# Kernel tuning notes

Hardware: AMD Instinct MI355X
Metric: run time of the kernel (lower is better)

## Reference

```python
import jax, jax.numpy as jnp
import numpy as np
from jax import lax

DIM = 192
HEADS = 6

def conv1x1(x, w, b):
    # x: [B,C,H,W], w: [O,C], b: [O]
    return jnp.einsum('oc,bchw->bohw', w, x) + b[None, :, None, None]

def dwconv3x3(x, w, b):
    # x: [B,C,H,W], w: [C,1,3,3] depthwise
    y = lax.conv_general_dilated(x, w, window_strides=(1, 1), padding='SAME',
                                 feature_group_count=x.shape[1],
                                 dimension_numbers=('NCHW', 'OIHW', 'NCHW'))
    return y + b[None, :, None, None]

def l2norm(x, eps=1e-12):
    # normalize along last axis (matches torch F.normalize)
    n = jnp.sqrt(jnp.sum(x * x, axis=-1, keepdims=True))
    return x / jnp.maximum(n, eps)

def setup_inputs() -> dict:
    key = jax.random.key(0)
    ks = jax.random.split(key, 12)
    b, c, h, w = 8, DIM, 128, 128
    s = 0.02
    return {
        'hsi': jax.random.normal(ks[0], (b, c, h, w), jnp.float32),
        'lidar': jax.random.normal(ks[1], (b, c, h, w), jnp.float32),
        'hsi_qv_w': jax.random.normal(ks[2], (2 * c, c), jnp.float32) * s,
        'hsi_qv_b': jnp.zeros((2 * c,), jnp.float32),
        'lidar_kv_w': jax.random.normal(ks[3], (2 * c, c), jnp.float32) * s,
        'lidar_kv_b': jnp.zeros((2 * c,), jnp.float32),
        'hsi_dw_w': jax.random.normal(ks[4], (2 * c, 1, 3, 3), jnp.float32) * s,
        'hsi_dw_b': jnp.zeros((2 * c,), jnp.float32),
        'lidar_dw_w': jax.random.normal(ks[5], (2 * c, 1, 3, 3), jnp.float32) * s,
        'lidar_dw_b': jnp.zeros((2 * c,), jnp.float32),
        'temperature': jnp.ones((HEADS, 1, 1), jnp.float32),
    }

def reference(hsi, lidar, hsi_qv_w, hsi_qv_b, lidar_kv_w, lidar_kv_b,
              hsi_dw_w, hsi_dw_b, lidar_dw_w, lidar_dw_b, temperature):
    b, c, h, w = hsi.shape
    hd = c // HEADS  # per-head channel dim
    hw = h * w

    hsi_qv = dwconv3x3(conv1x1(hsi, hsi_qv_w, hsi_qv_b), hsi_dw_w, hsi_dw_b)
    hsi_q, hsi_v = jnp.split(hsi_qv, 2, axis=1)
    lidar_kv = dwconv3x3(conv1x1(lidar, lidar_kv_w, lidar_kv_b), lidar_dw_w, lidar_dw_b)
    lidar_k, lidar_v = jnp.split(lidar_kv, 2, axis=1)

    def to_heads(x):  # [B,C,H,W] -> [B,head,hd,HW]
        return x.reshape(b, HEADS, hd, hw)

    q = l2norm(to_heads(hsi_q))
    k = l2norm(to_heads(lidar_k))
    v_h = to_heads(hsi_v)
    v_l = to_heads(lidar_v)

    attn = jnp.einsum('bncs,bnds->bncd', q, k) * temperature[None]  # [B,head,hd,hd]
    attn = jax.nn.softmax(attn, axis=-1)  # dropout is identity in eval mode

    hsi_out = jnp.einsum('bncd,bnds->bncs', attn, v_h) + v_h
    lidar_out = jnp.einsum('bncd,bnds->bncs', attn, v_l) + v_l

    hsi_out = hsi_out.reshape(b, c, h, w) + hsi
    lidar_out = lidar_out.reshape(b, c, h, w) + lidar
    return (hsi_out, lidar_out)
```

## Files before the change

kernel.cpp:

```cpp
#include <hip/hip_runtime.h>

typedef short v8s __attribute__((ext_vector_type(8)));
typedef float v4f __attribute__((ext_vector_type(4)));
typedef float v32f __attribute__((ext_vector_type(32)));

__device__ __forceinline__ unsigned short f2bf(float f){
  unsigned u = __builtin_bit_cast(unsigned, f);
  return (unsigned short)((u + 0x7fffu + ((u>>16)&1u)) >> 16);
}
__device__ __forceinline__ float bf2f(unsigned short s){
  return __builtin_bit_cast(float, ((unsigned)s) << 16);
}

__global__ __launch_bounds__(512) void k_conv1x1(
    const float* __restrict__ hsi, const float* __restrict__ lidar,
    const unsigned short* __restrict__ Wfrag, const float* __restrict__ hqb,
    const float* __restrict__ lkb, unsigned short* __restrict__ Sqk,
    unsigned short* __restrict__ Sv)
{
  const int bx   = blockIdx.x;
  const int tens = bx >> 11;
  const int nt   = bx & 2047;
  const int b    = nt >> 8;
  const int hw0  = (nt & 255) << 6;
  const float* X = (tens ? lidar : hsi) + ((size_t)b * 192) * 16384 + hw0;
  const float* bias = tens ? lkb : hqb;

  __shared__ unsigned short Xt[64][200];

  {
    const int c4   = (threadIdx.x & 15) * 4;
    const int krow = threadIdx.x >> 4;
    const float* xb2 = X + c4;
    float4 f[6];
    #pragma unroll
    for (int j = 0; j < 3; ++j){
      const int k = krow*2 + j*64;
      f[2*j]   = *(const float4*)(xb2 + (size_t)k * 16384);
      f[2*j+1] = *(const float4*)(xb2 + (size_t)(k+1) * 16384);
    }
    #pragma unroll
    for (int j = 0; j < 3; ++j){
      const int k = krow*2 + j*64;
      #pragma unroll
      for (int i2 = 0; i2 < 4; ++i2){
        const unsigned lo = f2bf(((const float*)&f[2*j])[i2]);
        const unsigned hi = f2bf(((const float*)&f[2*j+1])[i2]);
        *(unsigned*)&Xt[c4 + i2][k] = lo | (hi << 16);
      }
    }
  }
  __syncthreads();

  const int lane = threadIdx.x & 63;
  const int wid  = threadIdx.x >> 6;
  const int l15  = lane & 15;
  const int g    = lane >> 4;
  const int mstripe = wid * 48;
  const unsigned short* wb = Wfrag + ((size_t)(tens*8 + wid) * 18) * 512 + (lane << 3);

  v4f acc[3][4];
  #pragma unroll
  for (int i=0;i<3;i++)
    #pragma unroll
    for (int j=0;j<4;j++)
      acc[i][j] = (v4f){0.f,0.f,0.f,0.f};

  #pragma unroll
  for (int ks=0; ks<6; ++ks){
    const int k0 = ks*32;
    v8s af[3];
    #pragma unroll
    for (int mi=0; mi<3; ++mi)
      af[mi] = *(const v8s*)(wb + (size_t)(ks*3 + mi) * 512);
    #pragma unroll
    for (int ni=0; ni<4; ++ni){
      const v8s bfr = *(const v8s*)&Xt[ni*16 + l15][k0 + 8*g];
      #pragma unroll
      for (int mi=0; mi<3; ++mi)
        acc[mi][ni] = __builtin_amdgcn_mfma_f32_16x16x32_bf16(af[mi], bfr, acc[mi][ni], 0, 0, 0);
    }
  }

  unsigned short* outp;
  int cb;
  if (mstripe < 192){
    outp = Sqk + ((size_t)(tens*8 + b) * 192) * 16384 + hw0;
    cb = mstripe;
  } else {
    outp = Sv + ((size_t)(tens*8 + b) * 192) * 16384 + hw0;
    cb = mstripe - 192;
  }
  #pragma unroll
  for (int mi=0; mi<3; ++mi){
    #pragma unroll
    for (int r=0; r<4; ++r){
      const int co = mi*16 + 4*g + r;
      const float bs = bias[mstripe + co];
      #pragma unroll
      for (int ni=0; ni<4; ++ni)
        outp[(size_t)(cb + co)*16384 + ni*16 + l15] = f2bf(acc[mi][ni][r] + bs);
    }
  }
}

__global__ __launch_bounds__(256) void k_dw2(
    const unsigned short* __restrict__ Sqk, const unsigned short* __restrict__ Sv,
    const float* __restrict__ hdw, const float* __restrict__ ldw,
    const float* __restrict__ hdb, const float* __restrict__ ldb,
    unsigned short* __restrict__ QKd, unsigned short* __restrict__ Vb)
{
  const int bx = blockIdx.x;
  const int ytile = bx & 7;
  const int gp = bx >> 3;
  const int half = (gp >= 3072);
  const int p = half ? gp - 3072 : gp;
  const int tens = (p >= 1536);
  const int c = p % 192;
  const int woff = half ? 192 : 0;
  const unsigned short* in = (half ? Sv : Sqk) + (size_t)p*16384;
  unsigned short* out = (half ? Vb : QKd) + (size_t)p*16384;
  const int h0 = ytile*16;
  const int t = threadIdx.x;

  __shared__ __align__(16) unsigned short lds[18*136];

  #pragma unroll
  for (int it=0; it<2; ++it){
    const int slot = it*256 + t;
    if (slot < 288){
      const int row = slot >> 4;
      const int w16 = slot & 15;
      const int gr = h0 - 1 + row;
      v8s val = (v8s){0,0,0,0,0,0,0,0};
      if (gr >= 0 && gr < 128)
        val = *(const v8s*)(in + gr*128 + w16*8);
      *(v8s*)&lds[row*136 + w16*8] = val;
    }
  }
  __syncthreads();

  const int w8 = t & 15;
  const int hr = t >> 4;
  const int w0 = w8*8;

  float a9[3][10];
  #pragma unroll
  for (int dy=0; dy<3; ++dy){
    const unsigned short* rp = &lds[(hr + dy)*136];
    const v8s m = *(const v8s*)(rp + w0);
    #pragma unroll
    for (int j=0;j<8;++j) a9[dy][j+1] = bf2f((unsigned short)m[j]);
    a9[dy][0] = (w8 > 0)  ? bf2f(rp[w0-1]) : 0.f;
    a9[dy][9] = (w8 < 15) ? bf2f(rp[w0+8]) : 0.f;
  }

  const float* wp = (tens ? ldw : hdw) + (woff + c)*9;
  const float k00=wp[0],k01=wp[1],k02=wp[2],k10=wp[3],k11=wp[4],k12=wp[5],k20=wp[6],k21=wp[7],k22=wp[8];
  const float bs = (tens ? ldb : hdb)[woff + c];
  v8s o;
  #pragma unroll
  for (int j=0;j<8;++j){
    float a = bs
      + a9[0][j]*k00 + a9[0][j+1]*k01 + a9[0][j+2]*k02
      + a9[1][j]*k10 + a9[1][j+1]*k11 + a9[1][j+2]*k12
      + a9[2][j]*k20 + a9[2][j+1]*k21 + a9[2][j+2]*k22;
    o[j] = (short)f2bf(a);
  }
  *(v8s*)(out + (h0 + hr)*128 + w0) = o;
}

__global__ __launch_bounds__(256) void k_qk(
    const unsigned short* __restrict__ QKd, float* __restrict__ P)
{
  const int bh = blockIdx.x, split = blockIdx.y;
  const int lane = threadIdx.x & 63, wid = threadIdx.x >> 6;
  const int l15 = lane & 15, g = lane >> 4;
  const int b = bh/6, hd = bh%6;
  const unsigned short* qb = QKd + ((size_t)(0*8 + b)*192 + hd*32)*16384;
  const unsigned short* kb = QKd + ((size_t)(1*8 + b)*192 + hd*32)*16384;
  const int s0 = (split*4 + wid)*256;

  v4f aqk[2][2], aqq[2], akk[2];
  #pragma unroll
  for (int i=0;i<2;i++){
    aqq[i] = (v4f){0.f,0.f,0.f,0.f};
    akk[i] = (v4f){0.f,0.f,0.f,0.f};
    #pragma unroll
    for (int j=0;j<2;j++) aqk[i][j] = (v4f){0.f,0.f,0.f,0.f};
  }

  #pragma unroll
  for (int ks=0; ks<8; ++ks){
    const int s = s0 + ks*32 + 8*g;
    v8s qf[2], kf[2];
    #pragma unroll
    for (int mi=0;mi<2;++mi) qf[mi] = *(const v8s*)(qb + (size_t)(mi*16 + l15)*16384 + s);
    #pragma unroll
    for (int ni=0;ni<2;++ni) kf[ni] = *(const v8s*)(kb + (size_t)(ni*16 + l15)*16384 + s);
    #pragma unroll
    for (int mi=0;mi<2;++mi)
      #pragma unroll
      for (int ni=0;ni<2;++ni)
        aqk[mi][ni] = __builtin_amdgcn_mfma_f32_16x16x32_bf16(qf[mi], kf[ni], aqk[mi][ni],0,0,0);
    #pragma unroll
    for (int mi=0;mi<2;++mi){
      aqq[mi] = __builtin_amdgcn_mfma_f32_16x16x32_bf16(qf[mi], qf[mi], aqq[mi],0,0,0);
      akk[mi] = __builtin_amdgcn_mfma_f32_16x16x32_bf16(kf[mi], kf[mi], akk[mi],0,0,0);
    }
  }
  float* slot = P + ((size_t)bh*64 + split*4 + wid)*1088;
  #pragma unroll
  for (int mi=0;mi<2;++mi)
    #pragma unroll
    for (int ni=0;ni<2;++ni)
      #pragma unroll
      for (int r=0;r<4;++r)
        slot[(mi*16 + 4*g + r)*32 + ni*16 + l15] = aqk[mi][ni][r];
  #pragma unroll
  for (int mi=0;mi<2;++mi)
    #pragma unroll
    for (int r=0;r<4;++r)
      if (l15 == 4*g + r){
        slot[1024 + mi*16 + l15] = aqq[mi][r];
        slot[1056 + mi*16 + l15] = akk[mi][r];
      }
}

__global__ __launch_bounds__(256) void k_sm(
    const float* __restrict__ P, const float* __restrict__ temp, float* __restrict__ A)
{
  __shared__ float red[1088];
  const int bh = blockIdx.x, t = threadIdx.x;
  const float* base = P + (size_t)bh*64*1088;
  for (int i=t; i<1088; i+=256){
    float s = 0.f;
    for (int sl=0; sl<64; ++sl) s += base[(size_t)sl*1088 + i];
    red[i] = s;
  }
  __syncthreads();
  const int c = t >> 3, dq = t & 7;
  const float qn = fmaxf(sqrtf(red[1024+c]), 1e-12f);
  const float tp = temp[bh % 6];
  float v[4];
  #pragma unroll
  for (int r=0;r<4;++r){
    const int d = dq*4 + r;
    const float kn = fmaxf(sqrtf(red[1056+d]), 1e-12f);
    v[r] = red[c*32+d] / (qn*kn) * tp;
  }
  float mx = fmaxf(fmaxf(v[0],v[1]), fmaxf(v[2],v[3]));
  mx = fmaxf(mx, __shfl_xor(mx,1));
  mx = fmaxf(mx, __shfl_xor(mx,2));
  mx = fmaxf(mx, __shfl_xor(mx,4));
  float e[4]; float sum = 0.f;
  #pragma unroll
  for (int r=0;r<4;++r){ e[r] = __expf(v[r]-mx); sum += e[r]; }
  sum += __shfl_xor(sum,1); sum += __shfl_xor(sum,2); sum += __shfl_xor(sum,4);
  const float inv = 1.f/sum;
  #pragma unroll
  for (int r=0;r<4;++r){
    const int d = dq*4 + r;
    A[(size_t)bh*1024 + c*32 + d] = e[r]*inv + ((c == d) ? 1.f : 0.f);
  }
}

#define R32(M) M(0) M(1) M(2) M(3) M(4) M(5) M(6) M(7) M(8) M(9) M(10) M(11) M(12) M(13) M(14) M(15) \
               M(16) M(17) M(18) M(19) M(20) M(21) M(22) M(23) M(24) M(25) M(26) M(27) M(28) M(29) M(30) M(31)

__global__ __launch_bounds__(256) void k_out(
    const float* __restrict__ A, const unsigned short* __restrict__ Vb,
    const float* __restrict__ hsi, const float* __restrict__ lidar,
    float* __restrict__ outh, float* __restrict__ outl)
{
  const int tens = blockIdx.x & 1;
  const int bh = blockIdx.x >> 1;
  const int s = (blockIdx.y*256 + threadIdx.x)*2;
  const int b = bh/6, hd = bh%6;
  const float* Ab = A + (size_t)bh*1024;
  const unsigned short* V = Vb + ((size_t)(tens*8 + b)*192 + hd*32)*16384 + s;
  const float* X = (tens ? lidar : hsi) + ((size_t)b*192 + hd*32)*16384 + s;
  float* O = (tens ? outl : outh) + ((size_t)b*192 + hd*32)*16384 + s;

  v32f vx, vy;
#define LD_V(dd) { const unsigned u = *(const unsigned*)(V + (size_t)(dd)*16384); \
                   vx[dd] = bf2f((unsigned short)u); vy[dd] = bf2f((unsigned short)(u >> 16)); }
  R32(LD_V)
#undef LD_V

  for (int c=0; c<32; ++c){
    const float* Arow = Ab + c*32;
    const float2 x = *(const float2*)(X + (size_t)c*16384);
    float ax = x.x, ay = x.y;
#define FMA_D(dd) { const float a = Arow[dd]; ax += a*vx[dd]; ay += a*vy[dd]; }
    R32(FMA_D)
#undef FMA_D
    float2 o; o.x = ax; o.y = ay;
    *(float2*)(O + (size_t)c*16384) = o;
  }
}

__global__ __launch_bounds__(256) void k_wcvt(
    const float* __restrict__ a, const float* __restrict__ b, unsigned short* __restrict__ o)
{
  const int i = blockIdx.x*256 + threadIdx.x;
  if (i >= 147456) return;
  const int jj = i & 7;
  const int l  = (i >> 3) & 63;
  const int rest = i >> 9;
  const int mi = rest % 3;
  const int ks = (rest / 3) % 6;
  const int q  = rest / 18;
  const int wid = q & 7, tens = q >> 3;
  const int row = wid*48 + mi*16 + (l & 15);
  const int col = ks*32 + (l >> 4)*8 + jj;
  const float* src = tens ? b : a;
  o[i] = f2bf(src[row*192 + col]);
}

extern "C" void kernel_launch(void* const* d_in, const int* in_sizes, int n_in,
                              void* d_out, int out_size, void* d_ws, size_t ws_size,
                              hipStream_t stream) {
  const float* hsi   = (const float*)d_in[0];
  const float* lidar = (const float*)d_in[1];
  const float* hqw   = (const float*)d_in[2];
  const float* hqb   = (const float*)d_in[3];
  const float* lkw   = (const float*)d_in[4];
  const float* lkb   = (const float*)d_in[5];
  const float* hdw   = (const float*)d_in[6];
  const float* hdb   = (const float*)d_in[7];
  const float* ldw   = (const float*)d_in[8];
  const float* ldb   = (const float*)d_in[9];
  const float* temp  = (const float*)d_in[10];

  char* ws = (char*)d_ws;
  unsigned short* Sv  = (unsigned short*)(ws);
  unsigned short* Vb  = (unsigned short*)(ws + 100663296);
  unsigned short* Wbf = (unsigned short*)(ws + 201326592);
  float* P            = (float*)(ws + 201621504);
  float* A            = (float*)(ws + 214990848);

  float* outh = (float*)d_out;
  float* outl = outh + 25165824;
  unsigned short* Sqk = (unsigned short*)d_out;
  unsigned short* QKd = (unsigned short*)((char*)d_out + 100663296);

  k_wcvt<<<576, 256, 0, stream>>>(hqw, lkw, Wbf);
  k_conv1x1<<<4096, 512, 0, stream>>>(hsi, lidar, Wbf, hqb, lkb, Sqk, Sv);
  k_dw2<<<49152, 256, 0, stream>>>(Sqk, Sv, hdw, ldw, hdb, ldb, QKd, Vb);
  k_qk<<<dim3(48, 16), 256, 0, stream>>>(QKd, P);
  k_sm<<<48, 256, 0, stream>>>(P, temp, A);
  k_out<<<dim3(96, 32), 256, 0, stream>>>(A, Vb, hsi, lidar, outh, outl);
}
```

Before: 339.3 us.

## Fuse Q/K depthwise conv into QK Gram kernel, drop QKd round trip

The depthwise 3x3 conv for the Q and K halves is moved out of k_dw2 and computed on the fly inside the QK reduction kernel. Each block stages four rows of 32 Q and 32 K channels into swizzled LDS and reads halo rows from global memory. This removes writing and re-reading the QKd intermediate buffer (about 100 MB of bf16). In exchange, QK blocks now each process four image rows, the split grid doubles to 32, the partial buffer doubles to 128 slots per head, and k_sm sums twice as many partials. Halo rows are re-read from global memory with scalar loads.

```diff
diff --git a/kernel.cpp b/kernel.cpp
--- a/kernel.cpp
+++ b/kernel.cpp
@@ -105,21 +105,18 @@
 }
 
 __global__ __launch_bounds__(256) void k_dw2(
-    const unsigned short* __restrict__ Sqk, const unsigned short* __restrict__ Sv,
+    const unsigned short* __restrict__ Sv,
     const float* __restrict__ hdw, const float* __restrict__ ldw,
     const float* __restrict__ hdb, const float* __restrict__ ldb,
-    unsigned short* __restrict__ QKd, unsigned short* __restrict__ Vb)
+    unsigned short* __restrict__ Vb)
 {
   const int bx = blockIdx.x;
   const int ytile = bx & 7;
-  const int gp = bx >> 3;
-  const int half = (gp >= 3072);
-  const int p = half ? gp - 3072 : gp;
+  const int p = bx >> 3;
   const int tens = (p >= 1536);
   const int c = p % 192;
-  const int woff = half ? 192 : 0;
-  const unsigned short* in = (half ? Sv : Sqk) + (size_t)p*16384;
-  unsigned short* out = (half ? Vb : QKd) + (size_t)p*16384;
+  const unsigned short* in = Sv + (size_t)p*16384;
+  unsigned short* out = Vb + (size_t)p*16384;
   const int h0 = ytile*16;
   const int t = threadIdx.x;
 
@@ -155,9 +152,9 @@
     a9[dy][9] = (w8 < 15) ? bf2f(rp[w0+8]) : 0.f;
   }
 
-  const float* wp = (tens ? ldw : hdw) + (woff + c)*9;
+  const float* wp = (tens ? ldw : hdw) + (192 + c)*9;
   const float k00=wp[0],k01=wp[1],k02=wp[2],k10=wp[3],k11=wp[4],k12=wp[5],k20=wp[6],k21=wp[7],k22=wp[8];
-  const float bs = (tens ? ldb : hdb)[woff + c];
+  const float bs = (tens ? ldb : hdb)[192 + c];
   v8s o;
   #pragma unroll
   for (int j=0;j<8;++j){
@@ -170,16 +167,47 @@
   *(v8s*)(out + (h0 + hr)*128 + w0) = o;
 }
 
-__global__ __launch_bounds__(256) void k_qk(
-    const unsigned short* __restrict__ QKd, float* __restrict__ P)
+__global__ __launch_bounds__(256) void k_qkdw(
+    const unsigned short* __restrict__ Sqk, const float* __restrict__ hdw,
+    const float* __restrict__ ldw, const float* __restrict__ hdb,
+    const float* __restrict__ ldb, float* __restrict__ P)
 {
   const int bh = blockIdx.x, split = blockIdx.y;
   const int lane = threadIdx.x & 63, wid = threadIdx.x >> 6;
   const int l15 = lane & 15, g = lane >> 4;
   const int b = bh/6, hd = bh%6;
-  const unsigned short* qb = QKd + ((size_t)(0*8 + b)*192 + hd*32)*16384;
-  const unsigned short* kb = QKd + ((size_t)(1*8 + b)*192 + hd*32)*16384;
-  const int s0 = (split*4 + wid)*256;
+  const unsigned short* qpb = Sqk + ((size_t)b*192 + hd*32)*16384;
+  const unsigned short* kpb = Sqk + ((size_t)(8 + b)*192 + hd*32)*16384;
+  const int h0 = split*4;
+
+  __shared__ __align__(16) unsigned short T[32768];
+
+  {
+    const int t = threadIdx.x;
+    #pragma unroll
+    for (int i=0;i<16;++i){
+      const int seg = i*256 + t;
+      const int w16 = seg & 15;
+      const int row = (seg >> 4) & 3;
+      const int ch  = (seg >> 6) & 31;
+      const int tn  = seg >> 11;
+      const unsigned short* pl = (tn ? kpb : qpb) + (size_t)ch*16384;
+      const v8s val = *(const v8s*)(pl + (h0+row)*128 + w16*8);
+      *(v8s*)&T[(((tn*32+ch)*4+row)<<7) + ((w16 ^ (ch&7))<<3)] = val;
+    }
+  }
+  __syncthreads();
+
+  float wq[2][9], bq[2], wk[2][9], bk[2];
+  #pragma unroll
+  for (int mi=0; mi<2; ++mi){
+    const int c = hd*32 + mi*16 + l15;
+    #pragma unroll
+    for (int j=0;j<9;++j){ wq[mi][j] = hdw[c*9+j]; wk[mi][j] = ldw[c*9+j]; }
+    bq[mi] = hdb[c]; bk[mi] = ldb[c];
+  }
+
+  const int h = h0 + wid;
 
   v4f aqk[2][2], aqq[2], akk[2];
   #pragma unroll
@@ -191,13 +219,56 @@
   }
 
   #pragma unroll
-  for (int ks=0; ks<8; ++ks){
-    const int s = s0 + ks*32 + 8*g;
+  for (int ks=0; ks<4; ++ks){
+    const int w0 = ks*32 + 8*g;
     v8s qf[2], kf[2];
     #pragma unroll
-    for (int mi=0;mi<2;++mi) qf[mi] = *(const v8s*)(qb + (size_t)(mi*16 + l15)*16384 + s);
-    #pragma unroll
-    for (int ni=0;ni<2;++ni) kf[ni] = *(const v8s*)(kb + (size_t)(ni*16 + l15)*16384 + s);
+    for (int mi=0; mi<2; ++mi){
+      #pragma unroll
+      for (int qk=0; qk<2; ++qk){
+        const int ch = mi*16 + l15;
+        const unsigned short* pl = (qk ? kpb : qpb) + (size_t)ch*16384;
+        float a9[3][10];
+        #pragma unroll
+        for (int dy=0; dy<3; ++dy){
+          const int hh = h - 1 + dy;
+          const int lr = hh - h0;
+          if (lr >= 0 && lr < 4){
+            const int base = ((qk*32 + ch)*4 + lr) << 7;
+            const int wsw = (((w0 >> 3) ^ (ch & 7)) << 3);
+            const v8s m = *(const v8s*)&T[base + wsw];
+            #pragma unroll
+            for (int j=0;j<8;++j) a9[dy][j+1] = bf2f((unsigned short)m[j]);
+            a9[dy][0] = (w0 > 0)
+              ? bf2f(T[base + ((((w0-1)>>3) ^ (ch&7))<<3) + ((w0-1)&7)]) : 0.f;
+            a9[dy][9] = (w0 < 120)
+              ? bf2f(T[base + ((((w0+8)>>3) ^ (ch&7))<<3)]) : 0.f;
+          } else if (hh >= 0 && hh < 128){
+            const unsigned short* rp = pl + hh*128;
+            const v8s m = *(const v8s*)(rp + w0);
+            #pragma unroll
+            for (int j=0;j<8;++j) a9[dy][j+1] = bf2f((unsigned short)m[j]);
+            a9[dy][0] = (w0 > 0)   ? bf2f(rp[w0-1]) : 0.f;
+            a9[dy][9] = (w0 < 120) ? bf2f(rp[w0+8]) : 0.f;
+          } else {
+            #pragma unroll
+            for (int j=0;j<10;++j) a9[dy][j] = 0.f;
+          }
+        }
+        const float* w9 = qk ? wk[mi] : wq[mi];
+        const float bs = qk ? bk[mi] : bq[mi];
+        v8s o;
+        #pragma unroll
+        for (int j=0;j<8;++j){
+          float a = bs
+            + a9[0][j]*w9[0] + a9[0][j+1]*w9[1] + a9[0][j+2]*w9[2]
+            + a9[1][j]*w9[3] + a9[1][j+1]*w9[4] + a9[1][j+2]*w9[5]
+            + a9[2][j]*w9[6] + a9[2][j+1]*w9[7] + a9[2][j+2]*w9[8];
+          o[j] = (short)f2bf(a);
+        }
+        if (qk) kf[mi] = o; else qf[mi] = o;
+      }
+    }
     #pragma unroll
     for (int mi=0;mi<2;++mi)
       #pragma unroll
@@ -209,7 +280,7 @@
       akk[mi] = __builtin_amdgcn_mfma_f32_16x16x32_bf16(kf[mi], kf[mi], akk[mi],0,0,0);
     }
   }
-  float* slot = P + ((size_t)bh*64 + split*4 + wid)*1088;
+  float* slot = P + ((size_t)bh*128 + split*4 + wid)*1088;
   #pragma unroll
   for (int mi=0;mi<2;++mi)
     #pragma unroll
@@ -232,10 +303,10 @@
 {
   __shared__ float red[1088];
   const int bh = blockIdx.x, t = threadIdx.x;
-  const float* base = P + (size_t)bh*64*1088;
+  const float* base = P + (size_t)bh*128*1088;
   for (int i=t; i<1088; i+=256){
     float s = 0.f;
-    for (int sl=0; sl<64; ++sl) s += base[(size_t)sl*1088 + i];
+    for (int sl=0; sl<128; ++sl) s += base[(size_t)sl*1088 + i];
     red[i] = s;
   }
   __syncthreads();
@@ -338,17 +409,16 @@
   unsigned short* Vb  = (unsigned short*)(ws + 100663296);
   unsigned short* Wbf = (unsigned short*)(ws + 201326592);
   float* P            = (float*)(ws + 201621504);
-  float* A            = (float*)(ws + 214990848);
+  float* A            = (float*)(ws + 228360192);
 
   float* outh = (float*)d_out;
   float* outl = outh + 25165824;
   unsigned short* Sqk = (unsigned short*)d_out;
-  unsigned short* QKd = (unsigned short*)((char*)d_out + 100663296);
 
   k_wcvt<<<576, 256, 0, stream>>>(hqw, lkw, Wbf);
   k_conv1x1<<<4096, 512, 0, stream>>>(hsi, lidar, Wbf, hqb, lkb, Sqk, Sv);
-  k_dw2<<<49152, 256, 0, stream>>>(Sqk, Sv, hdw, ldw, hdb, ldb, QKd, Vb);
-  k_qk<<<dim3(48, 16), 256, 0, stream>>>(QKd, P);
+  k_dw2<<<24576, 256, 0, stream>>>(Sv, hdw, ldw, hdb, ldb, Vb);
+  k_qkdw<<<dim3(48, 32), 256, 0, stream>>>(Sqk, hdw, ldw, hdb, ldb, P);
   k_sm<<<48, 256, 0, stream>>>(P, temp, A);
   k_out<<<dim3(96, 32), 256, 0, stream>>>(A, Vb, hsi, lidar, outh, outl);
 }
```

Measured after the change: 373.4 us. 10.0% more time.
